# Performance work log

Hardware: AMD Instinct MI355X
Metric: run time of the kernel (lower is better)

## Reference

```python
import jax, jax.numpy as jnp
import numpy as np
from math import sqrt

DIM, RANK = 1024, 32
B, S = 4, 4096

def setup_inputs() -> dict:
    key = jax.random.key(0)
    kx, kq, kk, kv = jax.random.split(key, 4)
    # xavier_uniform bounds
    bq = sqrt(6.0 / (RANK + DIM))
    bv = sqrt(6.0 / (DIM + DIM))
    return {
        "x": jax.random.normal(kx, (B, S, DIM), dtype=jnp.float32),
        "Q": jax.random.uniform(kq, (RANK, DIM), jnp.float32, -bq, bq),
        "K": jax.random.uniform(kk, (RANK, DIM), jnp.float32, -bq, bq),
        "VO": jax.random.uniform(kv, (DIM, DIM), jnp.float32, -bv, bv),
    }

def reference(x, Q, K, VO):
    d = x.shape[-1]
    # low-rank projections: [b,t,r] each (avoid materializing QK^T [d,d] or 4-way einsum blowup)
    xq = jnp.einsum('btd,rd->btr', x, Q)
    xk = jnp.einsum('bud,rd->bur', x, K)
    scores = jnp.einsum('btr,bur->btu', xq, xk) / sqrt(d)
    attn = jax.nn.softmax(scores, axis=2)
    # value aggregation then output projection
    ctx = jnp.einsum('btu,bud->btd', attn, x)
    return jnp.einsum('btd,de->bte', ctx, VO)
```

## Files before the change

### kernel.cpp

```cpp
#include <hip/hip_runtime.h>
#include <hip/hip_bf16.h>

#define DIM  1024
#define RANK 32
#define BATCH 4
#define SEQ  4096
#define MTOT (BATCH * SEQ)

typedef short bf16x8 __attribute__((ext_vector_type(8)));
typedef float f32x4 __attribute__((ext_vector_type(4)));
typedef float f32x16 __attribute__((ext_vector_type(16)));
typedef unsigned short ushort8v __attribute__((ext_vector_type(8)));
typedef unsigned int uint2v __attribute__((ext_vector_type(2)));

__device__ inline unsigned short f2bf(float f) {
    union { float f; unsigned int u; } v; v.f = f;
    return (unsigned short)((v.u + 0x7FFFu + ((v.u >> 16) & 1u)) >> 16);
}

__device__ inline unsigned int pk_bf16(float a, float b) {
    __hip_bfloat162 h = __float22bfloat162_rn(make_float2(a, b));
    unsigned int u; __builtin_memcpy(&u, &h, 4);
    return u;
}

__device__ inline void gl_lds16(const unsigned short* g, unsigned short* l) {
    __builtin_amdgcn_global_load_lds(
        (const __attribute__((address_space(1))) unsigned int*)g,
        (__attribute__((address_space(3))) unsigned int*)l, 16, 0, 0);
}

__global__ __launch_bounds__(256) void k_cvt_qk(const float* __restrict__ Q,
                                                const float* __restrict__ K,
                                                unsigned short* __restrict__ wqk) {
    int i = blockIdx.x * 256 + threadIdx.x;
    int row = i >> 10, col = i & 1023;
    const float SC = 0.045084220027779984f;
    float v = (row < RANK) ? Q[row * DIM + col] * SC : K[(row - RANK) * DIM + col];
    wqk[i] = f2bf(v);
}

__global__ __launch_bounds__(256) void k_transpose_cvt(const float* __restrict__ in,
                                                       unsigned short* __restrict__ out,
                                                       int R, int C) {
    __shared__ float tile[64][65];
    const int tid = threadIdx.x;
    const int c0 = blockIdx.x * 64, r0 = blockIdx.y * 64;
    {
        int c = (tid & 15) * 4;
#pragma unroll
        for (int i = 0; i < 4; ++i) {
            int r = (tid >> 4) + i * 16;
            f32x4 v = *(const f32x4*)(in + (size_t)(r0 + r) * C + c0 + c);
            tile[r][c + 0] = v[0]; tile[r][c + 1] = v[1];
            tile[r][c + 2] = v[2]; tile[r][c + 3] = v[3];
        }
    }
    __syncthreads();
    {
        int r = (tid & 15) * 4;
#pragma unroll
        for (int i = 0; i < 4; ++i) {
            int c = (tid >> 4) + i * 16;
            unsigned short o0 = f2bf(tile[r + 0][c]), o1 = f2bf(tile[r + 1][c]);
            unsigned short o2 = f2bf(tile[r + 2][c]), o3 = f2bf(tile[r + 3][c]);
            unsigned short* p = out + (size_t)(c0 + c) * R + r0 + r;
            p[0] = o0; p[1] = o1; p[2] = o2; p[3] = o3;
        }
    }
}

__global__ __launch_bounds__(256) void k_xbf(const float* __restrict__ x,
                                             unsigned short* __restrict__ xbf) {
    size_t i = ((size_t)blockIdx.x * 256 + threadIdx.x) * 8;
    f32x4 v0 = *(const f32x4*)(x + i);
    f32x4 v1 = *(const f32x4*)(x + i + 4);
    ushort8v o;
    o[0] = f2bf(v0[0]); o[1] = f2bf(v0[1]); o[2] = f2bf(v0[2]); o[3] = f2bf(v0[3]);
    o[4] = f2bf(v1[0]); o[5] = f2bf(v1[1]); o[6] = f2bf(v1[2]); o[7] = f2bf(v1[3]);
    *(ushort8v*)(xbf + i) = o;
}

__global__ __launch_bounds__(256) void k_proj(const unsigned short* __restrict__ xbf,
                                              const unsigned short* __restrict__ wqk,
                                              unsigned short* __restrict__ xqk) {
    __shared__ __align__(16) unsigned short a_lds[128 * 32];
    __shared__ __align__(16) unsigned short w_lds[64 * 32];
    const int tid = threadIdx.x;
    const int w = tid >> 6, lane = tid & 63, l15 = lane & 15, quad = lane >> 4;
    const int wm = w & 1, wn = w >> 1;
    const int rowbase = blockIdx.x * 128;

    f32x4 acc[4][2];
#pragma unroll
    for (int mt = 0; mt < 4; ++mt)
#pragma unroll
        for (int nt = 0; nt < 2; ++nt) acc[mt][nt] = (f32x4){0.f, 0.f, 0.f, 0.f};

    const unsigned short* Ab = xbf + (size_t)(rowbase + w * 32 + (lane >> 2)) * DIM + (lane & 3) * 8;
    const unsigned short* Wb = wqk + (size_t)(w * 16 + (lane >> 2)) * DIM + (lane & 3) * 8;

    for (int k0 = 0; k0 < DIM; k0 += 32) {
        gl_lds16(Ab + k0, &a_lds[(w * 32) * 32]);
        gl_lds16(Ab + (size_t)16 * DIM + k0, &a_lds[(w * 32 + 16) * 32]);
        gl_lds16(Wb + k0, &w_lds[(w * 16) * 32]);
        __syncthreads();
        bf16x8 am[4], bn[2];
#pragma unroll
        for (int mt = 0; mt < 4; ++mt)
            am[mt] = *(const bf16x8*)&a_lds[(wm * 64 + mt * 16 + l15) * 32 + quad * 8];
#pragma unroll
        for (int nt = 0; nt < 2; ++nt)
            bn[nt] = *(const bf16x8*)&w_lds[(wn * 32 + nt * 16 + l15) * 32 + quad * 8];
#pragma unroll
        for (int mt = 0; mt < 4; ++mt)
#pragma unroll
            for (int nt = 0; nt < 2; ++nt)
                acc[mt][nt] = __builtin_amdgcn_mfma_f32_16x16x32_bf16(am[mt], bn[nt], acc[mt][nt], 0, 0, 0);
        __syncthreads();
    }
#pragma unroll
    for (int mt = 0; mt < 4; ++mt)
#pragma unroll
        for (int nt = 0; nt < 2; ++nt)
#pragma unroll
            for (int r = 0; r < 4; ++r) {
                int grow = rowbase + wm * 64 + mt * 16 + quad * 4 + r;
                xqk[(size_t)grow * 64 + wn * 32 + nt * 16 + l15] = f2bf(acc[mt][nt][r]);
            }
}

__global__ __launch_bounds__(256) void k_score(const unsigned short* __restrict__ xqk,
                                               unsigned short* __restrict__ P,
                                               float* __restrict__ den_part) {
    __shared__ __align__(16) unsigned short xk_lds[128 * 32];
    __shared__ __align__(16) unsigned short p_lds[64 * 136];
    __shared__ float denp[4][64];
    const int tid = threadIdx.x;
    const int w = tid >> 6, lane = tid & 63, l31 = lane & 31, half = lane >> 5;
    const int qbase = blockIdx.x * 64;
    const int kc = blockIdx.y;
    const int b = blockIdx.z;

    bf16x8 bq[2][2];
#pragma unroll
    for (int qt = 0; qt < 2; ++qt) {
        const unsigned short* base = xqk + (size_t)(b * SEQ + qbase + qt * 32 + l31) * 64 + half * 8;
        bq[qt][0] = *(const bf16x8*)(base);
        bq[qt][1] = *(const bf16x8*)(base + 16);
    }
    float dacc[2] = {0.f, 0.f};

    const unsigned short* XKb = xqk + (size_t)(b * SEQ + kc * 512 + w * 32 + (lane >> 2)) * 64 + 32 + (lane & 3) * 8;

    for (int it = 0; it < 4; ++it) {
        const int kkey = kc * 512 + it * 128;
        gl_lds16(XKb + (size_t)(it * 128) * 64, &xk_lds[(w * 32) * 32]);
        gl_lds16(XKb + (size_t)(it * 128 + 16) * 64, &xk_lds[(w * 32 + 16) * 32]);
        __syncthreads();

        bf16x8 ak0 = *(const bf16x8*)&xk_lds[(w * 32 + l31) * 32 + half * 8];
        bf16x8 ak1 = *(const bf16x8*)&xk_lds[(w * 32 + l31) * 32 + 16 + half * 8];
        f32x16 z;
#pragma unroll
        for (int i = 0; i < 16; ++i) z[i] = 0.f;
#pragma unroll
        for (int qt = 0; qt < 2; ++qt) {
            f32x16 sc = __builtin_amdgcn_mfma_f32_32x32x16_bf16(ak0, bq[qt][0], z, 0, 0, 0);
            sc = __builtin_amdgcn_mfma_f32_32x32x16_bf16(ak1, bq[qt][1], sc, 0, 0, 0);
#pragma unroll
            for (int g = 0; g < 4; ++g) {
                float e0 = exp2f(sc[4 * g + 0]), e1 = exp2f(sc[4 * g + 1]);
                float e2 = exp2f(sc[4 * g + 2]), e3 = exp2f(sc[4 * g + 3]);
                dacc[qt] += (e0 + e1) + (e2 + e3);
                uint2v dw; dw[0] = pk_bf16(e0, e1); dw[1] = pk_bf16(e2, e3);
                *(uint2v*)&p_lds[(qt * 32 + l31) * 136 + w * 32 + g * 8 + half * 4] = dw;
            }
        }
        __syncthreads();
#pragma unroll
        for (int i = 0; i < 4; ++i) {
            int row = i * 16 + (tid >> 4);
            int col = (tid & 15) * 8;
            ushort8v v = *(const ushort8v*)&p_lds[row * 136 + col];
            *(ushort8v*)(P + (size_t)(b * SEQ + qbase + row) * SEQ + kkey + col) = v;
        }
    }
#pragma unroll
    for (int qt = 0; qt < 2; ++qt) {
        float d = dacc[qt];
        d += __shfl_xor(d, 32);
        if (half == 0) denp[w][qt * 32 + l31] = d;
    }
    __syncthreads();
    if (tid < 64) {
        float s = denp[0][tid] + denp[1][tid] + denp[2][tid] + denp[3][tid];
        den_part[(size_t)kc * MTOT + b * SEQ + qbase + tid] = s;
    }
}

__global__ __launch_bounds__(512, 4) void k_xvo(const unsigned short* __restrict__ vot,
                                                const unsigned short* __restrict__ xbf,
                                                unsigned short* __restrict__ xvoT) {
    __shared__ __align__(16) unsigned short a_lds[128 * 64];
    __shared__ __align__(16) unsigned short b_lds[256 * 64];
    const int tid = threadIdx.x;
    const int w = tid >> 6, lane = tid & 63, l31 = lane & 31, half = lane >> 5;
    const int wm = w & 1, wn = w >> 1;
    const int ubase = blockIdx.x * 256;
    const int ebase = blockIdx.y * 128;
    const int b = blockIdx.z;

    f32x16 acc[2][2];
#pragma unroll
    for (int at = 0; at < 2; ++at)
#pragma unroll
        for (int bt = 0; bt < 2; ++bt)
#pragma unroll
            for (int i = 0; i < 16; ++i) acc[at][bt][i] = 0.f;

    const int sub = lane >> 3;
    const int g = (lane & 7) ^ (sub & 7);
    const int Ra = w * 16 + sub;
    const int Rb = w * 32 + sub;
    const unsigned short* Ap = vot + (size_t)(ebase + Ra) * DIM + g * 8;
    const unsigned short* Bp = xbf + (size_t)(b * SEQ + ubase + Rb) * DIM + g * 8;

    for (int k0 = 0; k0 < DIM; k0 += 64) {
#pragma unroll
        for (int c = 0; c < 2; ++c)
            gl_lds16(Ap + (size_t)(c * 8) * DIM + k0, &a_lds[(w * 16 + c * 8) * 64]);
#pragma unroll
        for (int c = 0; c < 4; ++c)
            gl_lds16(Bp + (size_t)(c * 8) * DIM + k0, &b_lds[(w * 32 + c * 8) * 64]);
        __syncthreads();

        const int abase = (wm * 64 + l31) * 64;
        const int bbase = (wn * 64 + l31) * 64;
#pragma unroll
        for (int ks = 0; ks < 4; ++ks) {
            const int soff = ((ks * 2 + half) ^ (l31 & 7)) * 8;
            bf16x8 a0 = *(const bf16x8*)&a_lds[abase + soff];
            bf16x8 a1 = *(const bf16x8*)&a_lds[abase + 2048 + soff];
            bf16x8 b0 = *(const bf16x8*)&b_lds[bbase + soff];
            bf16x8 b1 = *(const bf16x8*)&b_lds[bbase + 2048 + soff];
            acc[0][0] = __builtin_amdgcn_mfma_f32_32x32x16_bf16(a0, b0, acc[0][0], 0, 0, 0);
            acc[0][1] = __builtin_amdgcn_mfma_f32_32x32x16_bf16(a0, b1, acc[0][1], 0, 0, 0);
            acc[1][0] = __builtin_amdgcn_mfma_f32_32x32x16_bf16(a1, b0, acc[1][0], 0, 0, 0);
            acc[1][1] = __builtin_amdgcn_mfma_f32_32x32x16_bf16(a1, b1, acc[1][1], 0, 0, 0);
        }
        __syncthreads();
    }
#pragma unroll
    for (int at = 0; at < 2; ++at)
#pragma unroll
        for (int bt = 0; bt < 2; ++bt)
#pragma unroll
            for (int reg = 0; reg < 16; ++reg) {
                int lr = wm * 64 + at * 32 + (reg & 3) + 8 * (reg >> 2) + 4 * half;
                int u = ubase + wn * 64 + bt * 32 + l31;
                xvoT[(size_t)(b * DIM + ebase + lr) * SEQ + u] = f2bf(acc[at][bt][reg]);
            }
}

__global__ __launch_bounds__(512, 4) void k_pv(const unsigned short* __restrict__ P,
                                               const unsigned short* __restrict__ xvoT,
                                               const float* __restrict__ den_part,
                                               float* __restrict__ out) {
    __shared__ __align__(16) unsigned short a_lds[2][128 * 64];
    __shared__ __align__(16) unsigned short b_lds[256 * 64];
    __shared__ float rden[128];
    const int tid = threadIdx.x;
    const int w = tid >> 6, lane = tid & 63, l31 = lane & 31, half = lane >> 5;
    const int wm = w & 1, wn = w >> 1;

    const int p = blockIdx.x;
    const int xcd = p & 7, t0 = p >> 3;
    const int rowtile = xcd * 16 + (t0 >> 2);
    const int etile = t0 & 3;
    const int rowbase = rowtile * 128;
    const int ebase = etile * 256;
    const int b = rowbase >> 12;

    if (tid < 128) {
        float s = 0.f;
#pragma unroll
        for (int i = 0; i < 8; ++i) s += den_part[(size_t)i * MTOT + rowbase + tid];
        rden[tid] = 1.0f / s;
    }

    f32x16 acc[2][2];
#pragma unroll
    for (int at = 0; at < 2; ++at)
#pragma unroll
        for (int bt = 0; bt < 2; ++bt)
#pragma unroll
            for (int i = 0; i < 16; ++i) acc[at][bt][i] = 0.f;

    const int sub = lane >> 3;
    const int g = (lane & 7) ^ (sub & 7);
    const unsigned short* Ap = P + (size_t)(rowbase + w * 16 + sub) * SEQ + g * 8;
    const unsigned short* Bp = xvoT + (size_t)(b * DIM + ebase + w * 32 + sub) * SEQ + g * 8;

    auto stageA = [&](int sb, int k0) {
#pragma unroll
        for (int c = 0; c < 2; ++c)
            gl_lds16(Ap + (size_t)(c * 8) * SEQ + k0, &a_lds[sb][(w * 16 + c * 8) * 64]);
    };
    auto stageB = [&](int k0) {
#pragma unroll
        for (int c = 0; c < 4; ++c)
            gl_lds16(Bp + (size_t)(c * 8) * SEQ + k0, &b_lds[(w * 32 + c * 8) * 64]);
    };

    const int NT = SEQ / 64;
    stageA(0, 0);
    stageB(0);
    __syncthreads();

    int pb = 0;
    for (int t = 0; t < NT; ++t) {
        if (t + 1 < NT) stageA(pb ^ 1, (t + 1) * 64);

        const unsigned short* al = a_lds[pb];
        const int abase = (wm * 64 + l31) * 64;
        const int bbase = (wn * 64 + l31) * 64;
#pragma unroll
        for (int ks = 0; ks < 4; ++ks) {
            const int soff = ((ks * 2 + half) ^ (l31 & 7)) * 8;
            bf16x8 a0 = *(const bf16x8*)&al[abase + soff];
            bf16x8 a1 = *(const bf16x8*)&al[abase + 2048 + soff];
            bf16x8 b0 = *(const bf16x8*)&b_lds[bbase + soff];
            bf16x8 b1 = *(const bf16x8*)&b_lds[bbase + 2048 + soff];
            acc[0][0] = __builtin_amdgcn_mfma_f32_32x32x16_bf16(a0, b0, acc[0][0], 0, 0, 0);
            acc[0][1] = __builtin_amdgcn_mfma_f32_32x32x16_bf16(a0, b1, acc[0][1], 0, 0, 0);
            acc[1][0] = __builtin_amdgcn_mfma_f32_32x32x16_bf16(a1, b0, acc[1][0], 0, 0, 0);
            acc[1][1] = __builtin_amdgcn_mfma_f32_32x32x16_bf16(a1, b1, acc[1][1], 0, 0, 0);
        }
        asm volatile("s_waitcnt lgkmcnt(0)" ::: "memory");
        __builtin_amdgcn_s_barrier();
        asm volatile("" ::: "memory");

        if (t + 1 < NT) {
            stageB((t + 1) * 64);
            asm volatile("s_waitcnt vmcnt(0)" ::: "memory");
        }
        __builtin_amdgcn_s_barrier();
        asm volatile("" ::: "memory");
        pb ^= 1;
    }
#pragma unroll
    for (int at = 0; at < 2; ++at)
#pragma unroll
        for (int bt = 0; bt < 2; ++bt)
#pragma unroll
            for (int reg = 0; reg < 16; ++reg) {
                int lr = wm * 64 + at * 32 + (reg & 3) + 8 * (reg >> 2) + 4 * half;
                int e = ebase + wn * 64 + bt * 32 + l31;
                out[(size_t)(rowbase + lr) * DIM + e] = acc[at][bt][reg] * rden[lr];
            }
}

extern "C" void kernel_launch(void* const* d_in, const int* in_sizes, int n_in,
                              void* d_out, int out_size, void* d_ws, size_t ws_size,
                              hipStream_t stream) {
    const float* x  = (const float*)d_in[0];
    const float* Q  = (const float*)d_in[1];
    const float* K  = (const float*)d_in[2];
    const float* VO = (const float*)d_in[3];
    float* out = (float*)d_out;

    char* ws = (char*)d_ws;
    unsigned short* wqk  = (unsigned short*)(ws + 0);
    unsigned short* vot  = (unsigned short*)(ws + 131072);
    unsigned short* xqk  = (unsigned short*)(ws + 2228224);
    unsigned short* xbf  = (unsigned short*)(ws + 4325376);
    unsigned short* xvoT = (unsigned short*)(ws + 37879808);
    float*          denp = (float*)(ws + 71434240);
    unsigned short* P    = (unsigned short*)(ws + 71958528);

    k_cvt_qk<<<256, 256, 0, stream>>>(Q, K, wqk);
    k_transpose_cvt<<<dim3(16, 16, 1), 256, 0, stream>>>(VO, vot, 1024, 1024);
    k_xbf<<<8192, 256, 0, stream>>>(x, xbf);
    k_proj<<<128, 256, 0, stream>>>(xbf, wqk, xqk);
    k_score<<<dim3(SEQ / 64, 8, BATCH), 256, 0, stream>>>(xqk, P, denp);
    k_xvo<<<dim3(16, 8, BATCH), 512, 0, stream>>>(vot, xbf, xvoT);
    k_pv<<<dim3(512, 1, 1), 512, 0, stream>>>(P, xvoT, denp, out);
}
```

Before: 328.4 us.

## Fuse score/exp computation into PV kernel, eliminating materialized P matrix

Removes the separate score kernel that wrote the full bf16 probability matrix P (B*S*S) and partial denominators to global memory. The PV kernel now recomputes the exp'd scores per 64-key tile in-register via small MFMAs and writes them to a swizzled LDS tile, accumulating the row denominators locally. This trades a large HBM write and read of P for redundant score recomputation across the four e-tiles per row block. It also adds s_setprio around the main MFMA loop and register-prefetches the next key fragments.

```diff
diff --git a/kernel.cpp b/kernel.cpp
--- a/kernel.cpp
+++ b/kernel.cpp
@@ -128,75 +128,6 @@
                 int grow = rowbase + wm * 64 + mt * 16 + quad * 4 + r;
                 xqk[(size_t)grow * 64 + wn * 32 + nt * 16 + l15] = f2bf(acc[mt][nt][r]);
             }
-}
-
-__global__ __launch_bounds__(256) void k_score(const unsigned short* __restrict__ xqk,
-                                               unsigned short* __restrict__ P,
-                                               float* __restrict__ den_part) {
-    __shared__ __align__(16) unsigned short xk_lds[128 * 32];
-    __shared__ __align__(16) unsigned short p_lds[64 * 136];
-    __shared__ float denp[4][64];
-    const int tid = threadIdx.x;
-    const int w = tid >> 6, lane = tid & 63, l31 = lane & 31, half = lane >> 5;
-    const int qbase = blockIdx.x * 64;
-    const int kc = blockIdx.y;
-    const int b = blockIdx.z;
-
-    bf16x8 bq[2][2];
-#pragma unroll
-    for (int qt = 0; qt < 2; ++qt) {
-        const unsigned short* base = xqk + (size_t)(b * SEQ + qbase + qt * 32 + l31) * 64 + half * 8;
-        bq[qt][0] = *(const bf16x8*)(base);
-        bq[qt][1] = *(const bf16x8*)(base + 16);
-    }
-    float dacc[2] = {0.f, 0.f};
-
-    const unsigned short* XKb = xqk + (size_t)(b * SEQ + kc * 512 + w * 32 + (lane >> 2)) * 64 + 32 + (lane & 3) * 8;
-
-    for (int it = 0; it < 4; ++it) {
-        const int kkey = kc * 512 + it * 128;
-        gl_lds16(XKb + (size_t)(it * 128) * 64, &xk_lds[(w * 32) * 32]);
-        gl_lds16(XKb + (size_t)(it * 128 + 16) * 64, &xk_lds[(w * 32 + 16) * 32]);
-        __syncthreads();
-
-        bf16x8 ak0 = *(const bf16x8*)&xk_lds[(w * 32 + l31) * 32 + half * 8];
-        bf16x8 ak1 = *(const bf16x8*)&xk_lds[(w * 32 + l31) * 32 + 16 + half * 8];
-        f32x16 z;
-#pragma unroll
-        for (int i = 0; i < 16; ++i) z[i] = 0.f;
-#pragma unroll
-        for (int qt = 0; qt < 2; ++qt) {
-            f32x16 sc = __builtin_amdgcn_mfma_f32_32x32x16_bf16(ak0, bq[qt][0], z, 0, 0, 0);
-            sc = __builtin_amdgcn_mfma_f32_32x32x16_bf16(ak1, bq[qt][1], sc, 0, 0, 0);
-#pragma unroll
-            for (int g = 0; g < 4; ++g) {
-                float e0 = exp2f(sc[4 * g + 0]), e1 = exp2f(sc[4 * g + 1]);
-                float e2 = exp2f(sc[4 * g + 2]), e3 = exp2f(sc[4 * g + 3]);
-                dacc[qt] += (e0 + e1) + (e2 + e3);
-                uint2v dw; dw[0] = pk_bf16(e0, e1); dw[1] = pk_bf16(e2, e3);
-                *(uint2v*)&p_lds[(qt * 32 + l31) * 136 + w * 32 + g * 8 + half * 4] = dw;
-            }
-        }
-        __syncthreads();
-#pragma unroll
-        for (int i = 0; i < 4; ++i) {
-            int row = i * 16 + (tid >> 4);
-            int col = (tid & 15) * 8;
-            ushort8v v = *(const ushort8v*)&p_lds[row * 136 + col];
-            *(ushort8v*)(P + (size_t)(b * SEQ + qbase + row) * SEQ + kkey + col) = v;
-        }
-    }
-#pragma unroll
-    for (int qt = 0; qt < 2; ++qt) {
-        float d = dacc[qt];
-        d += __shfl_xor(d, 32);
-        if (half == 0) denp[w][qt * 32 + l31] = d;
-    }
-    __syncthreads();
-    if (tid < 64) {
-        float s = denp[0][tid] + denp[1][tid] + denp[2][tid] + denp[3][tid];
-        den_part[(size_t)kc * MTOT + b * SEQ + qbase + tid] = s;
-    }
 }
 
 __global__ __launch_bounds__(512, 4) void k_xvo(const unsigned short* __restrict__ vot,
@@ -263,16 +194,17 @@
             }
 }
 
-__global__ __launch_bounds__(512, 4) void k_pv(const unsigned short* __restrict__ P,
-                                               const unsigned short* __restrict__ xvoT,
-                                               const float* __restrict__ den_part,
-                                               float* __restrict__ out) {
-    __shared__ __align__(16) unsigned short a_lds[2][128 * 64];
+__global__ __launch_bounds__(512, 4) void k_spv(const unsigned short* __restrict__ xqk,
+                                                const unsigned short* __restrict__ xvoT,
+                                                float* __restrict__ out) {
+    __shared__ __align__(16) unsigned short p_lds[128 * 64];
     __shared__ __align__(16) unsigned short b_lds[256 * 64];
+    __shared__ float denp[8][32];
     __shared__ float rden[128];
     const int tid = threadIdx.x;
     const int w = tid >> 6, lane = tid & 63, l31 = lane & 31, half = lane >> 5;
     const int wm = w & 1, wn = w >> 1;
+    const int uu = w & 1, qq = w >> 1;
 
     const int p = blockIdx.x;
     const int xcd = p & 7, t0 = p >> 3;
@@ -282,12 +214,11 @@
     const int ebase = etile * 256;
     const int b = rowbase >> 12;
 
-    if (tid < 128) {
-        float s = 0.f;
-#pragma unroll
-        for (int i = 0; i < 8; ++i) s += den_part[(size_t)i * MTOT + rowbase + tid];
-        rden[tid] = 1.0f / s;
-    }
+    const unsigned short* xqp = xqk + (size_t)(rowbase + qq * 32 + l31) * 64 + half * 8;
+    const bf16x8 bq0 = *(const bf16x8*)(xqp);
+    const bf16x8 bq1 = *(const bf16x8*)(xqp + 16);
+
+    const unsigned short* xkp = xqk + (size_t)(b * SEQ + uu * 32 + l31) * 64 + 32 + half * 8;
 
     f32x16 acc[2][2];
 #pragma unroll
@@ -298,15 +229,8 @@
             for (int i = 0; i < 16; ++i) acc[at][bt][i] = 0.f;
 
     const int sub = lane >> 3;
-    const int g = (lane & 7) ^ (sub & 7);
-    const unsigned short* Ap = P + (size_t)(rowbase + w * 16 + sub) * SEQ + g * 8;
-    const unsigned short* Bp = xvoT + (size_t)(b * DIM + ebase + w * 32 + sub) * SEQ + g * 8;
-
-    auto stageA = [&](int sb, int k0) {
-#pragma unroll
-        for (int c = 0; c < 2; ++c)
-            gl_lds16(Ap + (size_t)(c * 8) * SEQ + k0, &a_lds[sb][(w * 16 + c * 8) * 64]);
-    };
+    const int g8 = (lane & 7) ^ (sub & 7);
+    const unsigned short* Bp = xvoT + (size_t)(b * DIM + ebase + w * 32 + sub) * SEQ + g8 * 8;
     auto stageB = [&](int k0) {
 #pragma unroll
         for (int c = 0; c < 4; ++c)
@@ -314,22 +238,47 @@
     };
 
     const int NT = SEQ / 64;
-    stageA(0, 0);
+    float dacc = 0.f;
+    const int pbase = (qq * 32 + l31) * 64 + half * 4;
+
     stageB(0);
-    __syncthreads();
-
-    int pb = 0;
+    bf16x8 kA0 = *(const bf16x8*)(xkp);
+    bf16x8 kA1 = *(const bf16x8*)(xkp + 16);
+    bf16x8 kB0, kB1;
+
     for (int t = 0; t < NT; ++t) {
-        if (t + 1 < NT) stageA(pb ^ 1, (t + 1) * 64);
-
-        const unsigned short* al = a_lds[pb];
+        f32x16 sc;
+#pragma unroll
+        for (int i = 0; i < 16; ++i) sc[i] = 0.f;
+        sc = __builtin_amdgcn_mfma_f32_32x32x16_bf16(kA0, bq0, sc, 0, 0, 0);
+        sc = __builtin_amdgcn_mfma_f32_32x32x16_bf16(kA1, bq1, sc, 0, 0, 0);
+#pragma unroll
+        for (int g = 0; g < 4; ++g) {
+            float e0 = exp2f(sc[4 * g + 0]), e1 = exp2f(sc[4 * g + 1]);
+            float e2 = exp2f(sc[4 * g + 2]), e3 = exp2f(sc[4 * g + 3]);
+            dacc += (e0 + e1) + (e2 + e3);
+            uint2v dw; dw[0] = pk_bf16(e0, e1); dw[1] = pk_bf16(e2, e3);
+            *(uint2v*)&p_lds[pbase + (((uu * 4 + g) ^ (l31 & 7)) * 8)] = dw;
+        }
+        asm volatile("s_waitcnt lgkmcnt(0)" ::: "memory");
+        asm volatile("s_waitcnt vmcnt(0)" ::: "memory");
+        __builtin_amdgcn_s_barrier();
+        asm volatile("" ::: "memory");
+
+        {
+            const unsigned short* nx = xkp + (size_t)((t + 1 < NT) ? (t + 1) : t) * 4096;
+            kB0 = *(const bf16x8*)(nx);
+            kB1 = *(const bf16x8*)(nx + 16);
+        }
+
         const int abase = (wm * 64 + l31) * 64;
         const int bbase = (wn * 64 + l31) * 64;
+        __builtin_amdgcn_s_setprio(1);
 #pragma unroll
         for (int ks = 0; ks < 4; ++ks) {
             const int soff = ((ks * 2 + half) ^ (l31 & 7)) * 8;
-            bf16x8 a0 = *(const bf16x8*)&al[abase + soff];
-            bf16x8 a1 = *(const bf16x8*)&al[abase + 2048 + soff];
+            bf16x8 a0 = *(const bf16x8*)&p_lds[abase + soff];
+            bf16x8 a1 = *(const bf16x8*)&p_lds[abase + 2048 + soff];
             bf16x8 b0 = *(const bf16x8*)&b_lds[bbase + soff];
             bf16x8 b1 = *(const bf16x8*)&b_lds[bbase + 2048 + soff];
             acc[0][0] = __builtin_amdgcn_mfma_f32_32x32x16_bf16(a0, b0, acc[0][0], 0, 0, 0);
@@ -337,18 +286,22 @@
             acc[1][0] = __builtin_amdgcn_mfma_f32_32x32x16_bf16(a1, b0, acc[1][0], 0, 0, 0);
             acc[1][1] = __builtin_amdgcn_mfma_f32_32x32x16_bf16(a1, b1, acc[1][1], 0, 0, 0);
         }
+        __builtin_amdgcn_s_setprio(0);
         asm volatile("s_waitcnt lgkmcnt(0)" ::: "memory");
         __builtin_amdgcn_s_barrier();
         asm volatile("" ::: "memory");
 
-        if (t + 1 < NT) {
-            stageB((t + 1) * 64);
-            asm volatile("s_waitcnt vmcnt(0)" ::: "memory");
-        }
-        __builtin_amdgcn_s_barrier();
-        asm volatile("" ::: "memory");
-        pb ^= 1;
-    }
+        if (t + 1 < NT) stageB((t + 1) * 64);
+        kA0 = kB0; kA1 = kB1;
+    }
+
+    dacc += __shfl_xor(dacc, 32);
+    if (half == 0) denp[w][l31] = dacc;
+    __syncthreads();
+    if (tid < 128)
+        rden[tid] = 1.0f / (denp[(tid >> 5) * 2][tid & 31] + denp[(tid >> 5) * 2 + 1][tid & 31]);
+    __syncthreads();
+
 #pragma unroll
     for (int at = 0; at < 2; ++at)
 #pragma unroll
@@ -376,14 +329,11 @@
     unsigned short* xqk  = (unsigned short*)(ws + 2228224);
     unsigned short* xbf  = (unsigned short*)(ws + 4325376);
     unsigned short* xvoT = (unsigned short*)(ws + 37879808);
-    float*          denp = (float*)(ws + 71434240);
-    unsigned short* P    = (unsigned short*)(ws + 71958528);
 
     k_cvt_qk<<<256, 256, 0, stream>>>(Q, K, wqk);
     k_transpose_cvt<<<dim3(16, 16, 1), 256, 0, stream>>>(VO, vot, 1024, 1024);
     k_xbf<<<8192, 256, 0, stream>>>(x, xbf);
     k_proj<<<128, 256, 0, stream>>>(xbf, wqk, xqk);
-    k_score<<<dim3(SEQ / 64, 8, BATCH), 256, 0, stream>>>(xqk, P, denp);
     k_xvo<<<dim3(16, 8, BATCH), 512, 0, stream>>>(vot, xbf, xvoT);
-    k_pv<<<dim3(512, 1, 1), 512, 0, stream>>>(P, xvoT, denp, out);
-}
+    k_spv<<<dim3(512, 1, 1), 512, 0, stream>>>(xqk, xvoT, out);
+}
```

Result: slower. 341.9 us (+4.1%).
